# Kernel tuning notes

Measured on AMD Instinct MI355X. Metric: run time of the kernel, lower is better.

Reference implementation:

```python
import jax, jax.numpy as jnp
import numpy as np

B, N, D, H = 4, 4096, 1024, 16
HD = D // H


def setup_inputs() -> dict:
    key = jax.random.key(0)
    k_x, k_qkv, k_proj, k_b = jax.random.split(key, 4)
    x = jax.random.normal(k_x, (B, N, D), dtype=jnp.float32)
    # torch nn.Linear weights: (out_features, in_features)
    w_qkv = jax.random.normal(k_qkv, (3 * D, D), dtype=jnp.float32) * (D ** -0.5)
    w_proj = jax.random.normal(k_proj, (D, D), dtype=jnp.float32) * (D ** -0.5)
    b_proj = jax.random.normal(k_b, (D,), dtype=jnp.float32) * 0.01
    return {"x": x, "w_qkv": w_qkv, "w_proj": w_proj, "b_proj": b_proj}


def reference(x, w_qkv, w_proj, b_proj):
    b, n, d = x.shape
    # qkv projection (no bias, qkv_bias=False)
    qkv = x @ w_qkv.T                       # (b, n, 3d)
    qkv = qkv.reshape(b, n, 3, H, HD)
    q, k, v = qkv[:, :, 0], qkv[:, :, 1], qkv[:, :, 2]   # each (b, n, H, HD)
    # Faithful to source: q @ k.transpose(-2,-1) with q,k of shape (b,n,H,HD)
    # -> per-token (H,H) attention across heads, softmax over last (head) axis.
    scale = HD ** -0.5
    attn = jnp.einsum('bnhd,bngd->bnhg', q, k) * scale   # (b, n, H, H)
    attn = jax.nn.softmax(attn, axis=-1)
    o = jnp.einsum('bnhg,bngd->bnhd', attn, v)           # (b, n, H, HD)
    # source: transpose(1,2).reshape(b,n,d) (contiguous copy then reshape)
    o = jnp.swapaxes(o, 1, 2).reshape(b, n, d)
    return o @ w_proj.T + b_proj
```

## Files before the change

### kernel.cpp

```cpp
#include <hip/hip_runtime.h>
#include <hip/hip_bf16.h>
#include <cstdint>
#include <cstddef>

#define NB      4
#define NSEQ    4096
#define DM      1024
#define NTOK    16384
#define QKV_N   3072

typedef __attribute__((ext_vector_type(8))) short short8_t;
typedef __attribute__((ext_vector_type(4))) short short4_t;
typedef __attribute__((ext_vector_type(4))) float f32x4;

static __device__ __forceinline__ unsigned short f2bf(float f) {
    unsigned u = __builtin_bit_cast(unsigned, f);
    u += 0x7fffu + ((u >> 16) & 1u);
    return (unsigned short)(u >> 16);
}

static __device__ __forceinline__ void async16(const void* g, void* l) {
    __builtin_amdgcn_global_load_lds(
        (const __attribute__((address_space(1))) void*)g,
        (__attribute__((address_space(3))) void*)l, 16, 0, 0);
}

__global__ void cvt_all(const float* __restrict__ x,
                        const float* __restrict__ wqkv,
                        const float* __restrict__ wproj,
                        unsigned short* __restrict__ xb,
                        unsigned short* __restrict__ wqkvb,
                        unsigned short* __restrict__ wprojb)
{
    int i = blockIdx.x * blockDim.x + threadIdx.x;
    const float* src; unsigned short* dst; int off;
    if (i < 4194304)      { src = x;     dst = xb;     off = i; }
    else if (i < 4980736) { src = wqkv;  dst = wqkvb;  off = i - 4194304; }
    else                  { src = wproj; dst = wprojb; off = i - 4980736; }
    float4 f = ((const float4*)src)[off];
    unsigned lo = (unsigned)f2bf(f.x) | ((unsigned)f2bf(f.y) << 16);
    unsigned hi = (unsigned)f2bf(f.z) | ((unsigned)f2bf(f.w) << 16);
    ((uint2*)dst)[off] = make_uint2(lo, hi);
}

template <bool BF16_OUT, bool BIAS>
__global__ __launch_bounds__(512, 2)
void gemm256(const unsigned short* __restrict__ A,
             const unsigned short* __restrict__ Bm,
             void* __restrict__ Cv,
             const float* __restrict__ bias,
             int M, int N, int K)
{
    __shared__ alignas(16) unsigned short As[2][16384];
    __shared__ alignas(16) unsigned short Bs[2][16384];

    const int t    = threadIdx.x;
    const int lane = t & 63;
    const int wave = t >> 6;
    const int quad = lane >> 4;
    const int r16  = lane & 15;
    const int wm   = wave >> 2;
    const int wn   = wave & 3;

    const int nwg = gridDim.x;
    const int swz = (blockIdx.x & 7) * (nwg >> 3) + (blockIdx.x >> 3);
    const int ntn = N >> 8;
    const int tm  = swz / ntn, tn = swz - tm * ntn;
    const int m0  = tm << 8, n0 = tn << 8;

    const int srow = t >> 3;
    const int schk = ((t & 7) ^ (srow & 7)) << 3;
    const unsigned short* gA = A  + (size_t)(m0 + srow) * K + schk;
    const unsigned short* gB = Bm + (size_t)(n0 + srow) * K + schk;
    unsigned short* const lA = &As[0][0] + t * 8;
    unsigned short* const lB = &Bs[0][0] + t * 8;

    const int NT = K >> 6;

#define STA(buf, kt, r) async16(gA + (size_t)(r) * 64 * K + (size_t)(kt) * 64, \
                                lA + (buf) * 16384 + (r) * 4096)
#define STB(buf, kt, r) async16(gB + (size_t)(r) * 64 * K + (size_t)(kt) * 64, \
                                lB + (buf) * 16384 + (r) * 4096)

    const int cs0 = ((quad    ) ^ (r16 & 7)) << 3;
    const int cs1 = ((quad ^ 4) ^ (r16 & 7)) << 3;
    const int aRow = wm * 128 + r16;
    const int bRow = wn * 64  + r16;

    f32x4 acc[8][4] = {};

#define RD_A(QR) _Pragma("unroll") for (int ii = 0; ii < 4; ++ii) {            \
        a[ii][0] = *(const short8_t*)(Ab + (aRow + (QR)*64 + ii*16) * 64 + cs0); \
        a[ii][1] = *(const short8_t*)(Ab + (aRow + (QR)*64 + ii*16) * 64 + cs1); }
#define RD_B(bb, QC) _Pragma("unroll") for (int jj = 0; jj < 2; ++jj) {        \
        bb[jj][0] = *(const short8_t*)(Bb + (bRow + (QC)*32 + jj*16) * 64 + cs0); \
        bb[jj][1] = *(const short8_t*)(Bb + (bRow + (QC)*32 + jj*16) * 64 + cs1); }
#define MM(QR, QC, bb) _Pragma("unroll") for (int s = 0; s < 2; ++s)           \
      _Pragma("unroll") for (int ii = 0; ii < 4; ++ii)                          \
        _Pragma("unroll") for (int jj = 0; jj < 2; ++jj)                        \
          acc[(QR)*4+ii][(QC)*2+jj] = __builtin_amdgcn_mfma_f32_16x16x32_bf16( \
              a[ii][s], bb[jj][s], acc[(QR)*4+ii][(QC)*2+jj], 0, 0, 0);
#define SYNC_PRE  __builtin_amdgcn_s_barrier();                                \
                  asm volatile("s_waitcnt lgkmcnt(0)" ::: "memory");           \
                  __builtin_amdgcn_sched_barrier(0);                           \
                  __builtin_amdgcn_s_setprio(1);
#define SYNC_POST __builtin_amdgcn_s_setprio(0);                               \
                  __builtin_amdgcn_s_barrier();                                \
                  asm volatile("" ::: "memory");

    STA(0,0,0); STA(0,0,1); STA(0,0,2); STA(0,0,3);
    STB(0,0,0); STB(0,0,1); STB(0,0,2); STB(0,0,3);
    STA(1,1,0); STA(1,1,1); STA(1,1,2); STA(1,1,3);
    STB(1,1,0); STB(1,1,1); STB(1,1,2); STB(1,1,3);
    asm volatile("s_waitcnt vmcnt(8)" ::: "memory");
    __builtin_amdgcn_s_barrier();

    for (int g = 0; g < NT; ++g) {
        const int cur = g & 1;
        const unsigned short* Ab = &As[cur][0];
        const unsigned short* Bb = &Bs[cur][0];
        const bool pf = (g + 2 < NT);
        short8_t a[4][2], b0[2][2], b1[2][2];

        RD_A(0) RD_B(b0, 0)
        SYNC_PRE
        MM(0, 0, b0)
        SYNC_POST

        RD_B(b1, 1)
        if (pf) { STA(cur, g+2, 0); STA(cur, g+2, 2); }
        SYNC_PRE
        MM(0, 1, b1)
        SYNC_POST

        RD_A(1)
        if (pf) { STB(cur, g+2, 0); STB(cur, g+2, 1); }
        SYNC_PRE
        MM(1, 0, b0)
        SYNC_POST

        if (pf) { STA(cur, g+2, 1); STA(cur, g+2, 3);
                  STB(cur, g+2, 2); STB(cur, g+2, 3); }
        __builtin_amdgcn_s_barrier();
        __builtin_amdgcn_s_setprio(1);
        MM(1, 1, b1)
        __builtin_amdgcn_s_setprio(0);
        if (pf)              asm volatile("s_waitcnt vmcnt(8)" ::: "memory");
        else if (g + 1 < NT) asm volatile("s_waitcnt vmcnt(0)" ::: "memory");
        __builtin_amdgcn_s_barrier();
        asm volatile("" ::: "memory");
    }

#undef STA
#undef STB
#undef RD_A
#undef RD_B
#undef MM
#undef SYNC_PRE
#undef SYNC_POST

    #pragma unroll
    for (int ri = 0; ri < 8; ++ri) {
        const int row = m0 + wm * 128 + (ri >> 2) * 64 + (ri & 3) * 16 + quad * 4;
        #pragma unroll
        for (int cj = 0; cj < 4; ++cj) {
            const int col = n0 + wn * 64 + (cj >> 1) * 32 + (cj & 1) * 16 + r16;
            float bv = 0.f;
            if constexpr (BIAS) bv = bias[col];
            #pragma unroll
            for (int r = 0; r < 4; ++r) {
                float v = acc[ri][cj][r] + bv;
                if constexpr (BF16_OUT)
                    ((unsigned short*)Cv)[(size_t)(row + r) * N + col] = f2bf(v);
                else
                    ((float*)Cv)[(size_t)(row + r) * N + col] = v;
            }
        }
    }
}

__global__ __launch_bounds__(256)
void attn_kernel(const unsigned short* __restrict__ qkv,
                 unsigned short* __restrict__ operm)
{
    __shared__ alignas(16) unsigned short s_qkv[4][QKV_N];
    __shared__ alignas(16) unsigned short s_p[4][256];
    __shared__ alignas(16) unsigned short s_o[4][16 * 72];
    const int t     = threadIdx.x;
    const int lane  = t & 63;
    const int wave  = t >> 6;
    const int quad  = lane >> 4;
    const int r16   = lane & 15;
    const int token = blockIdx.x * 4 + wave;

    {
        const unsigned short* src = qkv + (size_t)token * QKV_N;
        #pragma unroll
        for (int i = 0; i < 6; ++i)
            async16(src + i * 512 + lane * 8, &s_qkv[wave][i * 512 + lane * 8]);
    }
    asm volatile("s_waitcnt vmcnt(2)" ::: "memory");
    __builtin_amdgcn_sched_barrier(0);

    const unsigned short* q  = &s_qkv[wave][0];
    const unsigned short* kk = q + 1024;
    const unsigned short* vv = q + 2048;

    f32x4 s = {};
    #pragma unroll
    for (int c = 0; c < 64; c += 32) {
        short8_t aq = *(const short8_t*)(q  + r16 * 64 + c + quad * 8);
        short8_t bk = *(const short8_t*)(kk + r16 * 64 + c + quad * 8);
        s = __builtin_amdgcn_mfma_f32_16x16x32_bf16(aq, bk, s, 0, 0, 0);
    }

    #pragma unroll
    for (int r = 0; r < 4; ++r) {
        float x = s[r] * 0.125f;
        float m = x;
        #pragma unroll
        for (int o = 1; o < 16; o <<= 1) m = fmaxf(m, __shfl_xor(m, o));
        float e = __expf(x - m);
        float su = e;
        #pragma unroll
        for (int o = 1; o < 16; o <<= 1) su += __shfl_xor(su, o);
        s_p[wave][(quad * 4 + r) * 16 + r16] = f2bf(e * __builtin_amdgcn_rcpf(su));
    }

    asm volatile("s_waitcnt vmcnt(0)" ::: "memory");
    __builtin_amdgcn_sched_barrier(0);

    f32x4 o[4];
#if __has_builtin(__builtin_amdgcn_mfma_f32_16x16x16bf16_1k)
    short4_t pa = *(const short4_t*)(&s_p[wave][r16 * 16 + quad * 4]);
    #pragma unroll
    for (int j = 0; j < 4; ++j) {
        short4_t vb;
        #pragma unroll
        for (int e = 0; e < 4; ++e)
            vb[e] = (short)vv[(quad * 4 + e) * 64 + j * 16 + r16];
        f32x4 z = {};
        o[j] = __builtin_amdgcn_mfma_f32_16x16x16bf16_1k(pa, vb, z, 0, 0, 0);
    }
#else
    short8_t pa = {};
    if (quad < 2) pa = *(const short8_t*)(&s_p[wave][r16 * 16 + quad * 8]);
    #pragma unroll
    for (int j = 0; j < 4; ++j) {
        short8_t vb = {};
        if (quad < 2) {
            #pragma unroll
            for (int e = 0; e < 8; ++e)
                vb[e] = (short)vv[(quad * 8 + e) * 64 + j * 16 + r16];
        }
        f32x4 z = {};
        o[j] = __builtin_amdgcn_mfma_f32_16x16x32_bf16(pa, vb, z, 0, 0, 0);
    }
#endif

    #pragma unroll
    for (int j = 0; j < 4; ++j)
        #pragma unroll
        for (int r = 0; r < 4; ++r)
            s_o[wave][(quad * 4 + r) * 72 + j * 16 + r16] = f2bf(o[j][r]);

    const int b    = token >> 12;
    const int npos = token & 4095;
    const size_t base = (size_t)b * (NSEQ * DM)
                      + (size_t)(npos >> 4) * 1024
                      + (size_t)(npos & 15) * 64;
    #pragma unroll
    for (int c = lane; c < 128; c += 64) {
        const int h = c >> 3, part = c & 7;
        int4 val = *(const int4*)(&s_o[wave][h * 72 + part * 8]);
        *(int4*)(operm + base + (size_t)h * (256 * 1024) + part * 8) = val;
    }
}

extern "C" void kernel_launch(void* const* d_in, const int* in_sizes, int n_in,
                              void* d_out, int out_size, void* d_ws, size_t ws_size,
                              hipStream_t stream)
{
    const float* x      = (const float*)d_in[0];
    const float* w_qkv  = (const float*)d_in[1];
    const float* w_proj = (const float*)d_in[2];
    const float* b_proj = (const float*)d_in[3];
    float* out = (float*)d_out;

    unsigned short* xb     = (unsigned short*)d_ws;
    unsigned short* wqkvb  = xb     + (size_t)16777216;
    unsigned short* wprojb = wqkvb  + (size_t)3145728;
    unsigned short* qkvb   = wprojb + (size_t)1048576;
    unsigned short* opermb = qkvb   + (size_t)50331648;

    cvt_all<<<20480, 256, 0, stream>>>(x, w_qkv, w_proj, xb, wqkvb, wprojb);

    gemm256<true, false><<<768, 512, 0, stream>>>(xb, wqkvb, qkvb, nullptr,
                                                  NTOK, QKV_N, DM);

    attn_kernel<<<NTOK / 4, 256, 0, stream>>>(qkvb, opermb);

    gemm256<false, true><<<256, 512, 0, stream>>>(opermb, wprojb, out, b_proj,
                                                  NTOK, DM, DM);
}
```

Measured before the change: 303.5 us.

## Process eight tokens per wave in attention with double-buffered async prefetch

The attention kernel now has each wave loop over eight consecutive tokens. While the current token's Q/K/V sits in one LDS buffer, the next token's Q/K/V is prefetched into a second buffer through async global-to-LDS loads, with vmcnt waits tuned to each iteration. This is meant to hide global load latency and cut per-block launch overhead, at the cost of doubling LDS use for s_qkv, which may reduce occupancy. The fp32-to-bf16 conversion kernel also becomes grid-stride with a ten-times smaller grid.

```diff
diff --git a/kernel.cpp b/kernel.cpp
--- a/kernel.cpp
+++ b/kernel.cpp
@@ -8,6 +8,7 @@
 #define DM      1024
 #define NTOK    16384
 #define QKV_N   3072
+#define TPW     8
 
 typedef __attribute__((ext_vector_type(8))) short short8_t;
 typedef __attribute__((ext_vector_type(4))) short short4_t;
@@ -32,15 +33,17 @@
                         unsigned short* __restrict__ wqkvb,
                         unsigned short* __restrict__ wprojb)
 {
-    int i = blockIdx.x * blockDim.x + threadIdx.x;
-    const float* src; unsigned short* dst; int off;
-    if (i < 4194304)      { src = x;     dst = xb;     off = i; }
-    else if (i < 4980736) { src = wqkv;  dst = wqkvb;  off = i - 4194304; }
-    else                  { src = wproj; dst = wprojb; off = i - 4980736; }
-    float4 f = ((const float4*)src)[off];
-    unsigned lo = (unsigned)f2bf(f.x) | ((unsigned)f2bf(f.y) << 16);
-    unsigned hi = (unsigned)f2bf(f.z) | ((unsigned)f2bf(f.w) << 16);
-    ((uint2*)dst)[off] = make_uint2(lo, hi);
+    const int stride = gridDim.x * blockDim.x;
+    for (int i = blockIdx.x * blockDim.x + threadIdx.x; i < 5242880; i += stride) {
+        const float* src; unsigned short* dst; int off;
+        if (i < 4194304)      { src = x;     dst = xb;     off = i; }
+        else if (i < 4980736) { src = wqkv;  dst = wqkvb;  off = i - 4194304; }
+        else                  { src = wproj; dst = wprojb; off = i - 4980736; }
+        float4 f = ((const float4*)src)[off];
+        unsigned lo = (unsigned)f2bf(f.x) | ((unsigned)f2bf(f.y) << 16);
+        unsigned hi = (unsigned)f2bf(f.z) | ((unsigned)f2bf(f.w) << 16);
+        ((uint2*)dst)[off] = make_uint2(lo, hi);
+    }
 }
 
 template <bool BF16_OUT, bool BIAS>
@@ -183,7 +186,7 @@
 void attn_kernel(const unsigned short* __restrict__ qkv,
                  unsigned short* __restrict__ operm)
 {
-    __shared__ alignas(16) unsigned short s_qkv[4][QKV_N];
+    __shared__ alignas(16) unsigned short s_qkv[4][2][QKV_N];
     __shared__ alignas(16) unsigned short s_p[4][256];
     __shared__ alignas(16) unsigned short s_o[4][16 * 72];
     const int t     = threadIdx.x;
@@ -191,89 +194,102 @@
     const int wave  = t >> 6;
     const int quad  = lane >> 4;
     const int r16   = lane & 15;
-    const int token = blockIdx.x * 4 + wave;
+    const int tok0  = blockIdx.x * (4 * TPW) + wave * TPW;
 
     {
-        const unsigned short* src = qkv + (size_t)token * QKV_N;
+        const unsigned short* src = qkv + (size_t)tok0 * QKV_N;
         #pragma unroll
         for (int i = 0; i < 6; ++i)
-            async16(src + i * 512 + lane * 8, &s_qkv[wave][i * 512 + lane * 8]);
-    }
-    asm volatile("s_waitcnt vmcnt(2)" ::: "memory");
-    __builtin_amdgcn_sched_barrier(0);
-
-    const unsigned short* q  = &s_qkv[wave][0];
-    const unsigned short* kk = q + 1024;
-    const unsigned short* vv = q + 2048;
-
-    f32x4 s = {};
+            async16(src + i * 512 + lane * 8, &s_qkv[wave][0][i * 512 + lane * 8]);
+    }
+
     #pragma unroll
-    for (int c = 0; c < 64; c += 32) {
-        short8_t aq = *(const short8_t*)(q  + r16 * 64 + c + quad * 8);
-        short8_t bk = *(const short8_t*)(kk + r16 * 64 + c + quad * 8);
-        s = __builtin_amdgcn_mfma_f32_16x16x32_bf16(aq, bk, s, 0, 0, 0);
-    }
-
-    #pragma unroll
-    for (int r = 0; r < 4; ++r) {
-        float x = s[r] * 0.125f;
-        float m = x;
-        #pragma unroll
-        for (int o = 1; o < 16; o <<= 1) m = fmaxf(m, __shfl_xor(m, o));
-        float e = __expf(x - m);
-        float su = e;
-        #pragma unroll
-        for (int o = 1; o < 16; o <<= 1) su += __shfl_xor(su, o);
-        s_p[wave][(quad * 4 + r) * 16 + r16] = f2bf(e * __builtin_amdgcn_rcpf(su));
-    }
-
-    asm volatile("s_waitcnt vmcnt(0)" ::: "memory");
-    __builtin_amdgcn_sched_barrier(0);
-
-    f32x4 o[4];
+    for (int it = 0; it < TPW; ++it) {
+        const int buf   = it & 1;
+        const int token = tok0 + it;
+
+        if (it + 1 < TPW) {
+            const unsigned short* src = qkv + (size_t)(token + 1) * QKV_N;
+            #pragma unroll
+            for (int i = 0; i < 6; ++i)
+                async16(src + i * 512 + lane * 8,
+                        &s_qkv[wave][buf ^ 1][i * 512 + lane * 8]);
+        }
+        if (it == 0)           { asm volatile("s_waitcnt vmcnt(6)" ::: "memory"); }
+        else if (it + 1 < TPW) { asm volatile("s_waitcnt vmcnt(8)" ::: "memory"); }
+        else                   { asm volatile("s_waitcnt vmcnt(2)" ::: "memory"); }
+        __builtin_amdgcn_sched_barrier(0);
+
+        const unsigned short* q  = &s_qkv[wave][buf][0];
+        const unsigned short* kk = q + 1024;
+        const unsigned short* vv = q + 2048;
+
+        f32x4 s = {};
+        #pragma unroll
+        for (int c = 0; c < 64; c += 32) {
+            short8_t aq = *(const short8_t*)(q  + r16 * 64 + c + quad * 8);
+            short8_t bk = *(const short8_t*)(kk + r16 * 64 + c + quad * 8);
+            s = __builtin_amdgcn_mfma_f32_16x16x32_bf16(aq, bk, s, 0, 0, 0);
+        }
+
+        #pragma unroll
+        for (int r = 0; r < 4; ++r) {
+            float x = s[r] * 0.125f;
+            float m = x;
+            #pragma unroll
+            for (int o = 1; o < 16; o <<= 1) m = fmaxf(m, __shfl_xor(m, o));
+            float e = __expf(x - m);
+            float su = e;
+            #pragma unroll
+            for (int o = 1; o < 16; o <<= 1) su += __shfl_xor(su, o);
+            s_p[wave][(quad * 4 + r) * 16 + r16] = f2bf(e * __builtin_amdgcn_rcpf(su));
+        }
+
+        f32x4 o[4];
 #if __has_builtin(__builtin_amdgcn_mfma_f32_16x16x16bf16_1k)
-    short4_t pa = *(const short4_t*)(&s_p[wave][r16 * 16 + quad * 4]);
-    #pragma unroll
-    for (int j = 0; j < 4; ++j) {
-        short4_t vb;
-        #pragma unroll
-        for (int e = 0; e < 4; ++e)
-            vb[e] = (short)vv[(quad * 4 + e) * 64 + j * 16 + r16];
-        f32x4 z = {};
-        o[j] = __builtin_amdgcn_mfma_f32_16x16x16bf16_1k(pa, vb, z, 0, 0, 0);
-    }
+        short4_t pa = *(const short4_t*)(&s_p[wave][r16 * 16 + quad * 4]);
+        #pragma unroll
+        for (int j = 0; j < 4; ++j) {
+            short4_t vb;
+            #pragma unroll
+            for (int e = 0; e < 4; ++e)
+                vb[e] = (short)vv[(quad * 4 + e) * 64 + j * 16 + r16];
+            f32x4 z = {};
+            o[j] = __builtin_amdgcn_mfma_f32_16x16x16bf16_1k(pa, vb, z, 0, 0, 0);
+        }
 #else
-    short8_t pa = {};
-    if (quad < 2) pa = *(const short8_t*)(&s_p[wave][r16 * 16 + quad * 8]);
-    #pragma unroll
-    for (int j = 0; j < 4; ++j) {
-        short8_t vb = {};
-        if (quad < 2) {
-            #pragma unroll
-            for (int e = 0; e < 8; ++e)
-                vb[e] = (short)vv[(quad * 8 + e) * 64 + j * 16 + r16];
-        }
-        f32x4 z = {};
-        o[j] = __builtin_amdgcn_mfma_f32_16x16x32_bf16(pa, vb, z, 0, 0, 0);
-    }
+        short8_t pa = {};
+        if (quad < 2) pa = *(const short8_t*)(&s_p[wave][r16 * 16 + quad * 8]);
+        #pragma unroll
+        for (int j = 0; j < 4; ++j) {
+            short8_t vb = {};
+            if (quad < 2) {
+                #pragma unroll
+                for (int e = 0; e < 8; ++e)
+                    vb[e] = (short)vv[(quad * 8 + e) * 64 + j * 16 + r16];
+            }
+            f32x4 z = {};
+            o[j] = __builtin_amdgcn_mfma_f32_16x16x32_bf16(pa, vb, z, 0, 0, 0);
+        }
 #endif
 
-    #pragma unroll
-    for (int j = 0; j < 4; ++j)
-        #pragma unroll
-        for (int r = 0; r < 4; ++r)
-            s_o[wave][(quad * 4 + r) * 72 + j * 16 + r16] = f2bf(o[j][r]);
-
-    const int b    = token >> 12;
-    const int npos = token & 4095;
-    const size_t base = (size_t)b * (NSEQ * DM)
-                      + (size_t)(npos >> 4) * 1024
-                      + (size_t)(npos & 15) * 64;
-    #pragma unroll
-    for (int c = lane; c < 128; c += 64) {
-        const int h = c >> 3, part = c & 7;
-        int4 val = *(const int4*)(&s_o[wave][h * 72 + part * 8]);
-        *(int4*)(operm + base + (size_t)h * (256 * 1024) + part * 8) = val;
+        #pragma unroll
+        for (int j = 0; j < 4; ++j)
+            #pragma unroll
+            for (int r = 0; r < 4; ++r)
+                s_o[wave][(quad * 4 + r) * 72 + j * 16 + r16] = f2bf(o[j][r]);
+
+        const int b    = token >> 12;
+        const int npos = token & 4095;
+        const size_t base = (size_t)b * (NSEQ * DM)
+                          + (size_t)(npos >> 4) * 1024
+                          + (size_t)(npos & 15) * 64;
+        #pragma unroll
+        for (int c = lane; c < 128; c += 64) {
+            const int h = c >> 3, part = c & 7;
+            int4 val = *(const int4*)(&s_o[wave][h * 72 + part * 8]);
+            *(int4*)(operm + base + (size_t)h * (256 * 1024) + part * 8) = val;
+        }
     }
 }
 
@@ -293,12 +309,12 @@
     unsigned short* qkvb   = wprojb + (size_t)1048576;
     unsigned short* opermb = qkvb   + (size_t)50331648;
 
-    cvt_all<<<20480, 256, 0, stream>>>(x, w_qkv, w_proj, xb, wqkvb, wprojb);
+    cvt_all<<<2048, 256, 0, stream>>>(x, w_qkv, w_proj, xb, wqkvb, wprojb);
 
     gemm256<true, false><<<768, 512, 0, stream>>>(xb, wqkvb, qkvb, nullptr,
                                                   NTOK, QKV_N, DM);
 
-    attn_kernel<<<NTOK / 4, 256, 0, stream>>>(qkvb, opermb);
+    attn_kernel<<<NTOK / (4 * TPW), 256, 0, stream>>>(qkvb, opermb);
 
     gemm256<false, true><<<256, 512, 0, stream>>>(opermb, wprojb, out, b_proj,
                                                   NTOK, DM, DM);
```

Result: no change. 305.9 us (+0.8%).
